# Performance work log

Hardware: AMD Instinct MI355X
Metric: run time of the kernel (lower is better)

Reference implementation:

```python
import jax, jax.numpy as jnp
import numpy as np
import math

B, N, H = 4, 256, 256
D = H  # head_size == hidden_size since num_heads == 1
LN_EPS = 1e-5


def setup_inputs() -> dict:
    key = jax.random.key(0)
    ks = jax.random.split(key, 12)
    s = 0.02
    return {
        "hidden_states": jax.random.normal(ks[0], (B, N, H), jnp.float32),
        "structure_matrix": jax.random.normal(ks[1], (B, N, N, D), jnp.float32),
        "attention_mask": jnp.zeros((B, N), jnp.float32),
        # Linear weights stored as [in, out] (i.e., torch weight transposed)
        "Wq": jax.random.normal(ks[2], (D, D), jnp.float32) * s,
        "bq": jnp.zeros((D,), jnp.float32),
        "Wk": jax.random.normal(ks[3], (H, D), jnp.float32) * s,
        "bk": jnp.zeros((D,), jnp.float32),
        "Wv": jax.random.normal(ks[4], (D, D), jnp.float32) * s,
        "bv": jnp.zeros((D,), jnp.float32),
        "Wo": jax.random.normal(ks[5], (D, H), jnp.float32) * s,
        "bo": jnp.zeros((H,), jnp.float32),
        "ln_gamma": jnp.ones((H,), jnp.float32),
        "ln_beta": jnp.zeros((H,), jnp.float32),
    }


def _layer_norm(x, g, b):
    m = jnp.mean(x, axis=-1, keepdims=True)
    v = jnp.mean(jnp.square(x - m), axis=-1, keepdims=True)
    return g * (x - m) * jax.lax.rsqrt(v + LN_EPS) + b


def reference(hidden_states, structure_matrix, attention_mask,
              Wq, bq, Wk, bk, Wv, bv, Wo, bo, ln_gamma, ln_beta):
    # projections
    q = structure_matrix @ Wq + bq              # [B,L,R,D] with L=R=N
    k = hidden_states @ Wk + bk                 # [B,N,D]
    v = structure_matrix @ Wv + bv              # [B,L,R,D]
    Bq, L, R, Dh = q.shape
    # edge->node attention scores
    scores = jnp.einsum('blrd,bnd->blrn', q, k) / math.sqrt(Dh)
    scores = scores.reshape(Bq, L * R, -1)      # [B, N*N, N]
    # additive pairwise mask
    m2d = (attention_mask[:, :, None] * attention_mask[:, None, :]).reshape(Bq, -1)
    scores = scores + m2d[:, :, None]
    # relu + sum normalization (dropout = identity in eval mode)
    probs = jax.nn.relu(scores)
    probs = probs / jnp.sum(probs + 1e-12, axis=-1, keepdims=True)
    # aggregate edge values to nodes
    context = jnp.einsum('bmn,bmd->bnd', probs, v.reshape(Bq, L * R, Dh))
    out = context @ Wo + bo
    return _layer_norm(out + hidden_states, ln_gamma, ln_beta)
```

## Files before the change

kernel.cpp:

```cpp
#include <hip/hip_runtime.h>
#include <hip/hip_bf16.h>
#include <stdint.h>

#define NB 4
#define NN 256
#define DD 256
#define MM 65536

typedef __attribute__((ext_vector_type(8))) __bf16 bf16x8;
typedef __attribute__((ext_vector_type(4))) __bf16 bf16x4;
typedef __attribute__((ext_vector_type(4))) float f32x4;

__device__ __forceinline__ f32x4 mfma_bf16(bf16x8 a, bf16x8 b, f32x4 c) {
    return __builtin_amdgcn_mfma_f32_16x16x32_bf16(a, b, c, 0, 0, 0);
}

__device__ __forceinline__ size_t fragidx(int row, int col) {
    int nt = row >> 4, ln = row & 15;
    int kk = col >> 5, q = (col >> 3) & 3, e = col & 7;
    return ((size_t)((nt * 8 + kk) * 64 + q * 16 + ln)) * 8 + e;
}


__global__ void zero_kernel(float* __restrict__ p) {
    reinterpret_cast<float4*>(p)[blockIdx.x * 256 + threadIdx.x] =
        make_float4(0.f, 0.f, 0.f, 0.f);
}

__global__ void kkq_kernel(const float* __restrict__ hs, const float* __restrict__ Wk,
                           const float* __restrict__ bk, const float* __restrict__ Wq,
                           const float* __restrict__ bq, __bf16* __restrict__ kqf,
                           float* __restrict__ cb) {
    const int row = blockIdx.x, t = threadIdx.x;
    __shared__ float hr[256];
    __shared__ float kr[256];
    __shared__ float red[256];
    hr[t] = hs[(size_t)row * 256 + t];
    __syncthreads();
    float v = bk[t];
    for (int e = 0; e < 256; ++e)
        v = fmaf(hr[e], Wk[(size_t)e * 256 + t], v);
    kr[t] = v;
    red[t] = v * bq[t];
    __syncthreads();
    float u = 0.f;
    for (int d = 0; d < 256; ++d)
        u = fmaf(Wq[(size_t)t * 256 + d], kr[d], u);
    const int b = row >> 8, n = row & 255;
    kqf[(size_t)b * NN * DD + fragidx(n, t)] = (__bf16)(u * 0.0625f);
    for (int s = 128; s > 0; s >>= 1) {
        if (t < s) red[t] += red[t + s];
        __syncthreads();
    }
    if (t == 0) cb[row] = red[0] * 0.0625f;
}

__global__ void wvoprep_kernel(const float* __restrict__ Wv, const float* __restrict__ Wo,
                               const float* __restrict__ bv, __bf16* __restrict__ wvof,
                               float* __restrict__ bvo) {
    const int h = blockIdx.x, t = threadIdx.x;
    __shared__ float woc[256];
    __shared__ float red[256];
    float wo = Wo[(size_t)t * 256 + h];
    woc[t] = wo;
    red[t] = bv[t] * wo;
    __syncthreads();
    float v = 0.f;
    for (int d = 0; d < 256; ++d)
        v = fmaf(Wv[(size_t)t * 256 + d], woc[d], v);
    wvof[fragidx(h, t)] = (__bf16)v;
    for (int s = 128; s > 0; s >>= 1) {
        if (t < s) red[t] += red[t + s];
        __syncthreads();
    }
    if (t == 0) bvo[h] = red[0];
}

__global__ __launch_bounds__(256, 4)
void phaseA_kernel(const float* __restrict__ S, const __bf16* __restrict__ kqf,
                   const float* __restrict__ cb, const __bf16* __restrict__ wvof,
                   const float* __restrict__ bvo, const float* __restrict__ mask,
                   __bf16* __restrict__ PT, __bf16* __restrict__ VOT,
                   int c0, int CHS) {
    __shared__ __align__(16) __bf16 Tb[8 * 256 * 8];
    const int t = threadIdx.x;
    const int b = blockIdx.y;
    const int w = t >> 6;
    const int lane = t & 63;
    const int q = lane >> 4;
    const int ln = lane & 15;
    const int m0 = c0 + blockIdx.x * 64;
    const int mr = w * 16;

    const float* Ar = S + ((size_t)b * MM + m0 + mr + ln) * DD + q * 8;
    bf16x8 af[8];
#pragma unroll
    for (int kk = 0; kk < 8; ++kk) {
        float4 u0 = *reinterpret_cast<const float4*>(Ar + kk * 32);
        float4 u1 = *reinterpret_cast<const float4*>(Ar + kk * 32 + 4);
        af[kk] = (bf16x8){(__bf16)u0.x, (__bf16)u0.y, (__bf16)u0.z, (__bf16)u0.w,
                          (__bf16)u1.x, (__bf16)u1.y, (__bf16)u1.z, (__bf16)u1.w};
    }

    float m2[4];
#pragma unroll
    for (int r = 0; r < 4; ++r) {
        int mg = m0 + mr + q * 4 + r;
        m2[r] = mask[b * NN + (mg >> 8)] * mask[b * NN + (mg & 255)];
    }

    const int cblk = (mr >> 3) + (q >> 1);
    const int coff = (q & 1) * 4;
    float rs0 = 0.f, rs1 = 0.f, rs2 = 0.f, rs3 = 0.f;
    const __bf16* kqb = kqf + (size_t)b * NN * DD + (size_t)lane * 8;
    const float* cbb = cb + b * NN + ln;
#pragma unroll 2
    for (int nt = 0; nt < 16; ++nt) {
        f32x4 a = {0.f, 0.f, 0.f, 0.f};
        const __bf16* kr = kqb + (size_t)nt * 4096;
#pragma unroll
        for (int kk = 0; kk < 8; ++kk) {
            bf16x8 bf = *reinterpret_cast<const bf16x8*>(kr + kk * 512);
            a = mfma_bf16(af[kk], bf, a);
        }
        float cbv = cbb[nt * 16];
        a.x = fmaxf(a.x + cbv + m2[0], 0.f);
        a.y = fmaxf(a.y + cbv + m2[1], 0.f);
        a.z = fmaxf(a.z + cbv + m2[2], 0.f);
        a.w = fmaxf(a.w + cbv + m2[3], 0.f);
        rs0 += a.x; rs1 += a.y; rs2 += a.z; rs3 += a.w;
        bf16x4 pv = { (__bf16)a.x, (__bf16)a.y, (__bf16)a.z, (__bf16)a.w };
        *reinterpret_cast<bf16x4*>(&Tb[(size_t)(cblk * 256 + nt * 16 + ln) * 8 + coff]) = pv;
    }
#pragma unroll
    for (int off = 1; off < 16; off <<= 1) {
        rs0 += __shfl_xor(rs0, off);
        rs1 += __shfl_xor(rs1, off);
        rs2 += __shfl_xor(rs2, off);
        rs3 += __shfl_xor(rs3, off);
    }
    const float i0 = 1.f / (rs0 + 2.56e-10f);
    const float i1 = 1.f / (rs1 + 2.56e-10f);
    const float i2 = 1.f / (rs2 + 2.56e-10f);
    const float i3 = 1.f / (rs3 + 2.56e-10f);
    __syncthreads();

    {
        __bf16* Pg = PT + (size_t)b * NN * CHS + (size_t)(m0 - c0) * 256;
        const __bf16* Ts = Tb;
#pragma unroll
        for (int it = 0; it < 8; ++it) {
            int idx = it * 256 + t;
            *reinterpret_cast<bf16x8*>(Pg + (size_t)idx * 8) =
                *reinterpret_cast<const bf16x8*>(Ts + (size_t)idx * 8);
        }
    }
    __syncthreads();

    const __bf16* wvb = wvof + (size_t)lane * 8;
#pragma unroll 2
    for (int nt = 0; nt < 16; ++nt) {
        f32x4 a = {0.f, 0.f, 0.f, 0.f};
        const __bf16* wr = wvb + (size_t)nt * 4096;
#pragma unroll
        for (int kk = 0; kk < 8; ++kk) {
            bf16x8 bf = *reinterpret_cast<const bf16x8*>(wr + kk * 512);
            a = mfma_bf16(af[kk], bf, a);
        }
        float bb = bvo[nt * 16 + ln];
        bf16x4 pv = { (__bf16)((a.x + bb) * i0), (__bf16)((a.y + bb) * i1),
                      (__bf16)((a.z + bb) * i2), (__bf16)((a.w + bb) * i3) };
        *reinterpret_cast<bf16x4*>(&Tb[(size_t)(cblk * 256 + nt * 16 + ln) * 8 + coff]) = pv;
    }
    __syncthreads();
    {
        __bf16* Vg = VOT + (size_t)b * NN * CHS + (size_t)(m0 - c0) * 256;
        const __bf16* Ts = Tb;
#pragma unroll
        for (int it = 0; it < 8; ++it) {
            int idx = it * 256 + t;
            *reinterpret_cast<bf16x8*>(Vg + (size_t)idx * 8) =
                *reinterpret_cast<const bf16x8*>(Ts + (size_t)idx * 8);
        }
    }
}

__global__ __launch_bounds__(256, 2)
void phaseB_kernel(const __bf16* __restrict__ PT, const __bf16* __restrict__ VOT,
                   float* __restrict__ accg, int CHS) {
    const int t = threadIdx.x;
    const int b = blockIdx.z;
    const int w = t >> 6;
    const int lane = t & 63;
    const int q = lane >> 4;
    const int ln = lane & 15;
    const int n0 = (blockIdx.x >> 1) * 128 + (w >> 1) * 64;
    const int h0 = (blockIdx.x & 1) * 128 + (w & 1) * 64;
    const int g0 = blockIdx.y * 256;

    f32x4 acc[16];
#pragma unroll
    for (int i = 0; i < 16; ++i) acc[i] = (f32x4){0.f, 0.f, 0.f, 0.f};

    const __bf16* Pb = PT + (size_t)b * NN * CHS;
    const __bf16* Vb = VOT + (size_t)b * NN * CHS;
#pragma unroll 2
    for (int ks = 0; ks < 64; ++ks) {
        const __bf16* Pk = Pb + ((size_t)(g0 + ks * 4 + q) * 256 + n0 + ln) * 8;
        const __bf16* Vk = Vb + ((size_t)(g0 + ks * 4 + q) * 256 + h0 + ln) * 8;
        bf16x8 a[4], bb[4];
#pragma unroll
        for (int i = 0; i < 4; ++i)
            a[i] = *reinterpret_cast<const bf16x8*>(Pk + i * 128);
#pragma unroll
        for (int j = 0; j < 4; ++j)
            bb[j] = *reinterpret_cast<const bf16x8*>(Vk + j * 128);
#pragma unroll
        for (int i = 0; i < 4; ++i)
#pragma unroll
            for (int j = 0; j < 4; ++j)
                acc[i * 4 + j] = mfma_bf16(a[i], bb[j], acc[i * 4 + j]);
    }
    float* og = accg + (size_t)b * NN * DD;
#pragma unroll
    for (int i = 0; i < 4; ++i)
#pragma unroll
        for (int j = 0; j < 4; ++j) {
            f32x4 a = acc[i * 4 + j];
            int n = n0 + i * 16 + q * 4;
            int h = h0 + j * 16 + ln;
            atomicAdd(&og[(size_t)(n + 0) * DD + h], a.x);
            atomicAdd(&og[(size_t)(n + 1) * DD + h], a.y);
            atomicAdd(&og[(size_t)(n + 2) * DD + h], a.z);
            atomicAdd(&og[(size_t)(n + 3) * DD + h], a.w);
        }
}

__global__ void epilogue_kernel(const float* __restrict__ accg, const float* __restrict__ hs,
                                const float* __restrict__ bo, const float* __restrict__ g,
                                const float* __restrict__ be, float* __restrict__ out) {
    const int row = blockIdx.x, t = threadIdx.x;
    __shared__ float red[256];
    const size_t base = (size_t)row * 256;
    float x = accg[base + t] + bo[t] + hs[base + t];
    red[t] = x;
    __syncthreads();
    for (int s = 128; s > 0; s >>= 1) {
        if (t < s) red[t] += red[t + s];
        __syncthreads();
    }
    float mean = red[0] * (1.f / 256.f);
    __syncthreads();
    float d = x - mean;
    red[t] = d * d;
    __syncthreads();
    for (int s = 128; s > 0; s >>= 1) {
        if (t < s) red[t] += red[t + s];
        __syncthreads();
    }
    float var = red[0] * (1.f / 256.f);
    out[base + t] = g[t] * d * rsqrtf(var + 1e-5f) + be[t];
}

extern "C" void kernel_launch(void* const* d_in, const int* in_sizes, int n_in,
                              void* d_out, int out_size, void* d_ws, size_t ws_size,
                              hipStream_t stream) {
    const float* hs   = (const float*)d_in[0];
    const float* S    = (const float*)d_in[1];
    const float* mask = (const float*)d_in[2];
    const float* Wq   = (const float*)d_in[3];
    const float* bq   = (const float*)d_in[4];
    const float* Wk   = (const float*)d_in[5];
    const float* bk   = (const float*)d_in[6];
    const float* Wv   = (const float*)d_in[7];
    const float* bv   = (const float*)d_in[8];
    const float* Wo   = (const float*)d_in[9];
    const float* bo   = (const float*)d_in[10];
    const float* g    = (const float*)d_in[11];
    const float* be   = (const float*)d_in[12];
    float* out = (float*)d_out;

    char* ws = (char*)d_ws;
    size_t off = 0;
    auto alloc = [&](size_t bytes) {
        void* p = ws + off;
        off += (bytes + 255) & ~(size_t)255;
        return p;
    };
    float*  accg = (float*)alloc((size_t)NB * NN * DD * 4);
    __bf16* kqf  = (__bf16*)alloc((size_t)NB * NN * DD * 2);
    float*  cb   = (float*)alloc((size_t)NB * NN * 4);
    __bf16* wvof = (__bf16*)alloc((size_t)NN * DD * 2);
    float*  bvo  = (float*)alloc((size_t)NN * 4);
    size_t rem = ws_size > off ? ws_size - off : 0;
    int CH = MM;
    while (CH > 4096 && (size_t)CH * 4096 + 1024 > rem) CH >>= 1;
    __bf16* PT  = (__bf16*)alloc((size_t)NB * CH * NN * 2);
    __bf16* VOT = (__bf16*)alloc((size_t)NB * CH * NN * 2);

    zero_kernel<<<256, 256, 0, stream>>>(accg);
    kkq_kernel<<<NB * NN, 256, 0, stream>>>(hs, Wk, bk, Wq, bq, kqf, cb);
    wvoprep_kernel<<<NN, 256, 0, stream>>>(Wv, Wo, bv, wvof, bvo);
    for (int c0 = 0; c0 < MM; c0 += CH) {
        phaseA_kernel<<<dim3(CH / 64, NB), 256, 0, stream>>>(S, kqf, cb, wvof, bvo, mask,
                                                             PT, VOT, c0, CH);
        phaseB_kernel<<<dim3(4, CH / 2048, NB), 256, 0, stream>>>(PT, VOT, accg, CH);
    }
    epilogue_kernel<<<NB * NN, 256, 0, stream>>>(accg, hs, bo, g, be, out);
}
```

Before: 670.3 us.

## Give each phaseA wave four row tiles and store fragments directly

Each wave in phaseA now handles 64 rows (four 16-row MFMA tiles) instead of 16, so every loaded kqf/wvof B-fragment feeds four MFMAs. That cuts B-operand global/L2 traffic per row by a factor of four. The shared-memory staging buffer and its __syncthreads are dropped, and results are written straight to the PT/VOT global layout as 8-byte stores. In exchange, register use rises sharply (32 A-fragments plus 16 row sums), occupancy is lowered to 2 blocks, the grid shrinks by four, and the output stores are narrower and less coalesced.

```diff
diff --git a/kernel.cpp b/kernel.cpp
--- a/kernel.cpp
+++ b/kernel.cpp
@@ -76,112 +76,118 @@
     if (t == 0) bvo[h] = red[0];
 }
 
-__global__ __launch_bounds__(256, 4)
+__global__ __launch_bounds__(256, 2)
 void phaseA_kernel(const float* __restrict__ S, const __bf16* __restrict__ kqf,
                    const float* __restrict__ cb, const __bf16* __restrict__ wvof,
                    const float* __restrict__ bvo, const float* __restrict__ mask,
                    __bf16* __restrict__ PT, __bf16* __restrict__ VOT,
                    int c0, int CHS) {
-    __shared__ __align__(16) __bf16 Tb[8 * 256 * 8];
     const int t = threadIdx.x;
     const int b = blockIdx.y;
     const int w = t >> 6;
     const int lane = t & 63;
     const int q = lane >> 4;
     const int ln = lane & 15;
-    const int m0 = c0 + blockIdx.x * 64;
-    const int mr = w * 16;
-
-    const float* Ar = S + ((size_t)b * MM + m0 + mr + ln) * DD + q * 8;
-    bf16x8 af[8];
-#pragma unroll
-    for (int kk = 0; kk < 8; ++kk) {
-        float4 u0 = *reinterpret_cast<const float4*>(Ar + kk * 32);
-        float4 u1 = *reinterpret_cast<const float4*>(Ar + kk * 32 + 4);
-        af[kk] = (bf16x8){(__bf16)u0.x, (__bf16)u0.y, (__bf16)u0.z, (__bf16)u0.w,
-                          (__bf16)u1.x, (__bf16)u1.y, (__bf16)u1.z, (__bf16)u1.w};
-    }
-
-    float m2[4];
-#pragma unroll
-    for (int r = 0; r < 4; ++r) {
-        int mg = m0 + mr + q * 4 + r;
-        m2[r] = mask[b * NN + (mg >> 8)] * mask[b * NN + (mg & 255)];
-    }
-
-    const int cblk = (mr >> 3) + (q >> 1);
-    const int coff = (q & 1) * 4;
-    float rs0 = 0.f, rs1 = 0.f, rs2 = 0.f, rs3 = 0.f;
+    const int mloc = blockIdx.x * 256 + w * 64;
+    const int m0 = c0 + mloc;
+
+    bf16x8 af[4][8];
+#pragma unroll
+    for (int mt = 0; mt < 4; ++mt) {
+        const float* Ar = S + ((size_t)b * MM + m0 + mt * 16 + ln) * DD + q * 8;
+#pragma unroll
+        for (int kk = 0; kk < 8; ++kk) {
+            float4 u0 = *reinterpret_cast<const float4*>(Ar + kk * 32);
+            float4 u1 = *reinterpret_cast<const float4*>(Ar + kk * 32 + 4);
+            af[mt][kk] = (bf16x8){(__bf16)u0.x, (__bf16)u0.y, (__bf16)u0.z, (__bf16)u0.w,
+                                  (__bf16)u1.x, (__bf16)u1.y, (__bf16)u1.z, (__bf16)u1.w};
+        }
+    }
+
+    float m2[16];
+#pragma unroll
+    for (int mt = 0; mt < 4; ++mt)
+#pragma unroll
+        for (int r = 0; r < 4; ++r) {
+            int mg = m0 + mt * 16 + q * 4 + r;
+            m2[mt * 4 + r] = mask[b * NN + (mg >> 8)] * mask[b * NN + (mg & 255)];
+        }
+
+    float rs[16];
+#pragma unroll
+    for (int i = 0; i < 16; ++i) rs[i] = 0.f;
+
     const __bf16* kqb = kqf + (size_t)b * NN * DD + (size_t)lane * 8;
     const float* cbb = cb + b * NN + ln;
+    __bf16* Pb = PT + (size_t)b * NN * CHS;
+    __bf16* Vb = VOT + (size_t)b * NN * CHS;
+    const int mb0 = mloc >> 3;
+    const size_t so = (size_t)ln * 8 + (size_t)(q & 1) * 4;
+
 #pragma unroll 2
     for (int nt = 0; nt < 16; ++nt) {
-        f32x4 a = {0.f, 0.f, 0.f, 0.f};
+        f32x4 a0 = {0.f, 0.f, 0.f, 0.f}, a1 = a0, a2 = a0, a3 = a0;
         const __bf16* kr = kqb + (size_t)nt * 4096;
 #pragma unroll
         for (int kk = 0; kk < 8; ++kk) {
             bf16x8 bf = *reinterpret_cast<const bf16x8*>(kr + kk * 512);
-            a = mfma_bf16(af[kk], bf, a);
-        }
-        float cbv = cbb[nt * 16];
-        a.x = fmaxf(a.x + cbv + m2[0], 0.f);
-        a.y = fmaxf(a.y + cbv + m2[1], 0.f);
-        a.z = fmaxf(a.z + cbv + m2[2], 0.f);
-        a.w = fmaxf(a.w + cbv + m2[3], 0.f);
-        rs0 += a.x; rs1 += a.y; rs2 += a.z; rs3 += a.w;
-        bf16x4 pv = { (__bf16)a.x, (__bf16)a.y, (__bf16)a.z, (__bf16)a.w };
-        *reinterpret_cast<bf16x4*>(&Tb[(size_t)(cblk * 256 + nt * 16 + ln) * 8 + coff]) = pv;
-    }
-#pragma unroll
-    for (int off = 1; off < 16; off <<= 1) {
-        rs0 += __shfl_xor(rs0, off);
-        rs1 += __shfl_xor(rs1, off);
-        rs2 += __shfl_xor(rs2, off);
-        rs3 += __shfl_xor(rs3, off);
-    }
-    const float i0 = 1.f / (rs0 + 2.56e-10f);
-    const float i1 = 1.f / (rs1 + 2.56e-10f);
-    const float i2 = 1.f / (rs2 + 2.56e-10f);
-    const float i3 = 1.f / (rs3 + 2.56e-10f);
-    __syncthreads();
-
-    {
-        __bf16* Pg = PT + (size_t)b * NN * CHS + (size_t)(m0 - c0) * 256;
-        const __bf16* Ts = Tb;
-#pragma unroll
-        for (int it = 0; it < 8; ++it) {
-            int idx = it * 256 + t;
-            *reinterpret_cast<bf16x8*>(Pg + (size_t)idx * 8) =
-                *reinterpret_cast<const bf16x8*>(Ts + (size_t)idx * 8);
-        }
-    }
-    __syncthreads();
+            a0 = mfma_bf16(af[0][kk], bf, a0);
+            a1 = mfma_bf16(af[1][kk], bf, a1);
+            a2 = mfma_bf16(af[2][kk], bf, a2);
+            a3 = mfma_bf16(af[3][kk], bf, a3);
+        }
+        const float cbv = cbb[nt * 16];
+#define PROC_S(mt, A)                                                              \
+        {                                                                          \
+            float x0 = fmaxf(A.x + cbv + m2[mt * 4 + 0], 0.f);                     \
+            float x1 = fmaxf(A.y + cbv + m2[mt * 4 + 1], 0.f);                     \
+            float x2 = fmaxf(A.z + cbv + m2[mt * 4 + 2], 0.f);                     \
+            float x3 = fmaxf(A.w + cbv + m2[mt * 4 + 3], 0.f);                     \
+            rs[mt * 4 + 0] += x0; rs[mt * 4 + 1] += x1;                            \
+            rs[mt * 4 + 2] += x2; rs[mt * 4 + 3] += x3;                            \
+            bf16x4 pv = {(__bf16)x0, (__bf16)x1, (__bf16)x2, (__bf16)x3};          \
+            *reinterpret_cast<bf16x4*>(Pb + (size_t)(mb0 + mt * 2 + (q >> 1)) * 2048 \
+                                       + (size_t)nt * 128 + so) = pv;              \
+        }
+        PROC_S(0, a0) PROC_S(1, a1) PROC_S(2, a2) PROC_S(3, a3)
+#undef PROC_S
+    }
+
+#pragma unroll
+    for (int i = 0; i < 16; ++i) {
+        float v = rs[i];
+        v += __shfl_xor(v, 1);
+        v += __shfl_xor(v, 2);
+        v += __shfl_xor(v, 4);
+        v += __shfl_xor(v, 8);
+        rs[i] = 1.f / (v + 2.56e-10f);
+    }
 
     const __bf16* wvb = wvof + (size_t)lane * 8;
 #pragma unroll 2
     for (int nt = 0; nt < 16; ++nt) {
-        f32x4 a = {0.f, 0.f, 0.f, 0.f};
+        f32x4 a0 = {0.f, 0.f, 0.f, 0.f}, a1 = a0, a2 = a0, a3 = a0;
         const __bf16* wr = wvb + (size_t)nt * 4096;
 #pragma unroll
         for (int kk = 0; kk < 8; ++kk) {
             bf16x8 bf = *reinterpret_cast<const bf16x8*>(wr + kk * 512);
-            a = mfma_bf16(af[kk], bf, a);
-        }
-        float bb = bvo[nt * 16 + ln];
-        bf16x4 pv = { (__bf16)((a.x + bb) * i0), (__bf16)((a.y + bb) * i1),
-                      (__bf16)((a.z + bb) * i2), (__bf16)((a.w + bb) * i3) };
-        *reinterpret_cast<bf16x4*>(&Tb[(size_t)(cblk * 256 + nt * 16 + ln) * 8 + coff]) = pv;
-    }
-    __syncthreads();
-    {
-        __bf16* Vg = VOT + (size_t)b * NN * CHS + (size_t)(m0 - c0) * 256;
-        const __bf16* Ts = Tb;
-#pragma unroll
-        for (int it = 0; it < 8; ++it) {
-            int idx = it * 256 + t;
-            *reinterpret_cast<bf16x8*>(Vg + (size_t)idx * 8) =
-                *reinterpret_cast<const bf16x8*>(Ts + (size_t)idx * 8);
-        }
+            a0 = mfma_bf16(af[0][kk], bf, a0);
+            a1 = mfma_bf16(af[1][kk], bf, a1);
+            a2 = mfma_bf16(af[2][kk], bf, a2);
+            a3 = mfma_bf16(af[3][kk], bf, a3);
+        }
+        const float bb = bvo[nt * 16 + ln];
+#define PROC_V(mt, A)                                                              \
+        {                                                                          \
+            bf16x4 pv = {(__bf16)((A.x + bb) * rs[mt * 4 + 0]),                    \
+                         (__bf16)((A.y + bb) * rs[mt * 4 + 1]),                    \
+                         (__bf16)((A.z + bb) * rs[mt * 4 + 2]),                    \
+                         (__bf16)((A.w + bb) * rs[mt * 4 + 3])};                   \
+            *reinterpret_cast<bf16x4*>(Vb + (size_t)(mb0 + mt * 2 + (q >> 1)) * 2048 \
+                                       + (size_t)nt * 128 + so) = pv;              \
+        }
+        PROC_V(0, a0) PROC_V(1, a1) PROC_V(2, a2) PROC_V(3, a3)
+#undef PROC_V
     }
 }
 
@@ -302,8 +308,8 @@
     kkq_kernel<<<NB * NN, 256, 0, stream>>>(hs, Wk, bk, Wq, bq, kqf, cb);
     wvoprep_kernel<<<NN, 256, 0, stream>>>(Wv, Wo, bv, wvof, bvo);
     for (int c0 = 0; c0 < MM; c0 += CH) {
-        phaseA_kernel<<<dim3(CH / 64, NB), 256, 0, stream>>>(S, kqf, cb, wvof, bvo, mask,
-                                                             PT, VOT, c0, CH);
+        phaseA_kernel<<<dim3(CH / 256, NB), 256, 0, stream>>>(S, kqf, cb, wvof, bvo, mask,
+                                                              PT, VOT, c0, CH);
         phaseB_kernel<<<dim3(4, CH / 2048, NB), 256, 0, stream>>>(PT, VOT, accg, CH);
     }
     epilogue_kernel<<<NB * NN, 256, 0, stream>>>(accg, hs, bo, g, be, out);
```

Result: faster. 641.8 us (-4.2%).

## Aggregate raw structure matrix and apply fused Wv·Wo projection after reduction

Applied to the files above, without the earlier changes.

Phase A no longer multiplies each edge row by the fused Wv·Wo matrix. It writes a bf16 transposed copy of the structure matrix plus normalized probabilities, and accumulates per-node probability sums for the bias term. The fused projection then runs once per node in the epilogue as a 256x256 fp32 matvec, which removes half of the per-edge MFMA work. The costs are a strided transposing gather of S in phase A, atomics for the probability sums, a heavier epilogue, and a smaller default chunk size that launches the kernel loop twice.

```diff
diff --git a/kernel.cpp b/kernel.cpp
--- a/kernel.cpp
+++ b/kernel.cpp
@@ -56,7 +56,7 @@
 }
 
 __global__ void wvoprep_kernel(const float* __restrict__ Wv, const float* __restrict__ Wo,
-                               const float* __restrict__ bv, __bf16* __restrict__ wvof,
+                               const float* __restrict__ bv, float* __restrict__ wvo,
                                float* __restrict__ bvo) {
     const int h = blockIdx.x, t = threadIdx.x;
     __shared__ float woc[256];
@@ -68,7 +68,7 @@
     float v = 0.f;
     for (int d = 0; d < 256; ++d)
         v = fmaf(Wv[(size_t)t * 256 + d], woc[d], v);
-    wvof[fragidx(h, t)] = (__bf16)v;
+    wvo[(size_t)h * 256 + t] = v;
     for (int s = 128; s > 0; s >>= 1) {
         if (t < s) red[t] += red[t + s];
         __syncthreads();
@@ -76,24 +76,23 @@
     if (t == 0) bvo[h] = red[0];
 }
 
-__global__ __launch_bounds__(256, 4)
+__global__ __launch_bounds__(256, 3)
 void phaseA_kernel(const float* __restrict__ S, const __bf16* __restrict__ kqf,
-                   const float* __restrict__ cb, const __bf16* __restrict__ wvof,
-                   const float* __restrict__ bvo, const float* __restrict__ mask,
-                   __bf16* __restrict__ PT, __bf16* __restrict__ VOT,
-                   int c0, int CHS) {
-    __shared__ __align__(16) __bf16 Tb[8 * 256 * 8];
+                   const float* __restrict__ cb, const float* __restrict__ mask,
+                   __bf16* __restrict__ PT, __bf16* __restrict__ ST,
+                   float* __restrict__ wg, int c0, int CHS) {
     const int t = threadIdx.x;
     const int b = blockIdx.y;
     const int w = t >> 6;
     const int lane = t & 63;
     const int q = lane >> 4;
     const int ln = lane & 15;
-    const int m0 = c0 + blockIdx.x * 64;
-    const int mr = w * 16;
-
-    const float* Ar = S + ((size_t)b * MM + m0 + mr + ln) * DD + q * 8;
+    const int mloc = blockIdx.x * 64 + w * 16;
+    const int m0 = c0 + mloc;
+    const int mb0 = mloc >> 3;
+
     bf16x8 af[8];
+    const float* Ar = S + ((size_t)b * MM + m0 + ln) * DD + q * 8;
 #pragma unroll
     for (int kk = 0; kk < 8; ++kk) {
         float4 u0 = *reinterpret_cast<const float4*>(Ar + kk * 32);
@@ -102,19 +101,31 @@
                           (__bf16)u1.x, (__bf16)u1.y, (__bf16)u1.z, (__bf16)u1.w};
     }
 
+    __bf16* Sb = ST + (size_t)b * NN * CHS;
+#pragma unroll
+    for (int it = 0; it < 8; ++it) {
+        const int aa = it >> 2;
+        const int d = (it & 3) * 64 + lane;
+        const float* Sr = S + ((size_t)b * MM + m0 + aa * 8) * DD + d;
+        bf16x8 sv = {(__bf16)Sr[0],      (__bf16)Sr[DD],     (__bf16)Sr[2 * DD],
+                     (__bf16)Sr[3 * DD], (__bf16)Sr[4 * DD], (__bf16)Sr[5 * DD],
+                     (__bf16)Sr[6 * DD], (__bf16)Sr[7 * DD]};
+        *reinterpret_cast<bf16x8*>(Sb + ((size_t)(mb0 + aa) * 256 + d) * 8) = sv;
+    }
+
     float m2[4];
 #pragma unroll
     for (int r = 0; r < 4; ++r) {
-        int mg = m0 + mr + q * 4 + r;
+        int mg = m0 + q * 4 + r;
         m2[r] = mask[b * NN + (mg >> 8)] * mask[b * NN + (mg & 255)];
     }
 
-    const int cblk = (mr >> 3) + (q >> 1);
-    const int coff = (q & 1) * 4;
-    float rs0 = 0.f, rs1 = 0.f, rs2 = 0.f, rs3 = 0.f;
     const __bf16* kqb = kqf + (size_t)b * NN * DD + (size_t)lane * 8;
     const float* cbb = cb + b * NN + ln;
-#pragma unroll 2
+
+    f32x4 p[16];
+    float rs0 = 0.f, rs1 = 0.f, rs2 = 0.f, rs3 = 0.f;
+#pragma unroll
     for (int nt = 0; nt < 16; ++nt) {
         f32x4 a = {0.f, 0.f, 0.f, 0.f};
         const __bf16* kr = kqb + (size_t)nt * 4096;
@@ -123,14 +134,13 @@
             bf16x8 bf = *reinterpret_cast<const bf16x8*>(kr + kk * 512);
             a = mfma_bf16(af[kk], bf, a);
         }
-        float cbv = cbb[nt * 16];
+        const float cbv = cbb[nt * 16];
         a.x = fmaxf(a.x + cbv + m2[0], 0.f);
         a.y = fmaxf(a.y + cbv + m2[1], 0.f);
         a.z = fmaxf(a.z + cbv + m2[2], 0.f);
         a.w = fmaxf(a.w + cbv + m2[3], 0.f);
         rs0 += a.x; rs1 += a.y; rs2 += a.z; rs3 += a.w;
-        bf16x4 pv = { (__bf16)a.x, (__bf16)a.y, (__bf16)a.z, (__bf16)a.w };
-        *reinterpret_cast<bf16x4*>(&Tb[(size_t)(cblk * 256 + nt * 16 + ln) * 8 + coff]) = pv;
+        p[nt] = a;
     }
 #pragma unroll
     for (int off = 1; off < 16; off <<= 1) {
@@ -143,50 +153,24 @@
     const float i1 = 1.f / (rs1 + 2.56e-10f);
     const float i2 = 1.f / (rs2 + 2.56e-10f);
     const float i3 = 1.f / (rs3 + 2.56e-10f);
-    __syncthreads();
-
-    {
-        __bf16* Pg = PT + (size_t)b * NN * CHS + (size_t)(m0 - c0) * 256;
-        const __bf16* Ts = Tb;
-#pragma unroll
-        for (int it = 0; it < 8; ++it) {
-            int idx = it * 256 + t;
-            *reinterpret_cast<bf16x8*>(Pg + (size_t)idx * 8) =
-                *reinterpret_cast<const bf16x8*>(Ts + (size_t)idx * 8);
-        }
-    }
-    __syncthreads();
-
-    const __bf16* wvb = wvof + (size_t)lane * 8;
-#pragma unroll 2
+
+    __bf16* Pb = PT + (size_t)b * NN * CHS;
+    const size_t so = (size_t)ln * 8 + (size_t)(q & 1) * 4;
+#pragma unroll
     for (int nt = 0; nt < 16; ++nt) {
-        f32x4 a = {0.f, 0.f, 0.f, 0.f};
-        const __bf16* wr = wvb + (size_t)nt * 4096;
-#pragma unroll
-        for (int kk = 0; kk < 8; ++kk) {
-            bf16x8 bf = *reinterpret_cast<const bf16x8*>(wr + kk * 512);
-            a = mfma_bf16(af[kk], bf, a);
-        }
-        float bb = bvo[nt * 16 + ln];
-        bf16x4 pv = { (__bf16)((a.x + bb) * i0), (__bf16)((a.y + bb) * i1),
-                      (__bf16)((a.z + bb) * i2), (__bf16)((a.w + bb) * i3) };
-        *reinterpret_cast<bf16x4*>(&Tb[(size_t)(cblk * 256 + nt * 16 + ln) * 8 + coff]) = pv;
-    }
-    __syncthreads();
-    {
-        __bf16* Vg = VOT + (size_t)b * NN * CHS + (size_t)(m0 - c0) * 256;
-        const __bf16* Ts = Tb;
-#pragma unroll
-        for (int it = 0; it < 8; ++it) {
-            int idx = it * 256 + t;
-            *reinterpret_cast<bf16x8*>(Vg + (size_t)idx * 8) =
-                *reinterpret_cast<const bf16x8*>(Ts + (size_t)idx * 8);
-        }
+        float x0 = p[nt].x * i0, x1 = p[nt].y * i1, x2 = p[nt].z * i2, x3 = p[nt].w * i3;
+        bf16x4 pv = {(__bf16)x0, (__bf16)x1, (__bf16)x2, (__bf16)x3};
+        *reinterpret_cast<bf16x4*>(Pb + (size_t)(mb0 + (q >> 1)) * 2048
+                                   + (size_t)nt * 128 + so) = pv;
+        float wn = x0 + x1 + x2 + x3;
+        wn += __shfl_xor(wn, 16);
+        wn += __shfl_xor(wn, 32);
+        if (q == 0) atomicAdd(&wg[b * NN + nt * 16 + ln], wn);
     }
 }
 
 __global__ __launch_bounds__(256, 2)
-void phaseB_kernel(const __bf16* __restrict__ PT, const __bf16* __restrict__ VOT,
+void phaseB_kernel(const __bf16* __restrict__ PT, const __bf16* __restrict__ ST,
                    float* __restrict__ accg, int CHS) {
     const int t = threadIdx.x;
     const int b = blockIdx.z;
@@ -203,7 +187,7 @@
     for (int i = 0; i < 16; ++i) acc[i] = (f32x4){0.f, 0.f, 0.f, 0.f};
 
     const __bf16* Pb = PT + (size_t)b * NN * CHS;
-    const __bf16* Vb = VOT + (size_t)b * NN * CHS;
+    const __bf16* Vb = ST + (size_t)b * NN * CHS;
 #pragma unroll 2
     for (int ks = 0; ks < 64; ++ks) {
         const __bf16* Pk = Pb + ((size_t)(g0 + ks * 4 + q) * 256 + n0 + ln) * 8;
@@ -236,13 +220,22 @@
         }
 }
 
-__global__ void epilogue_kernel(const float* __restrict__ accg, const float* __restrict__ hs,
-                                const float* __restrict__ bo, const float* __restrict__ g,
-                                const float* __restrict__ be, float* __restrict__ out) {
+__global__ void epilogue_kernel(const float* __restrict__ Gg, const float* __restrict__ wg,
+                                const float* __restrict__ wvo, const float* __restrict__ bvo,
+                                const float* __restrict__ hs, const float* __restrict__ bo,
+                                const float* __restrict__ g, const float* __restrict__ be,
+                                float* __restrict__ out) {
     const int row = blockIdx.x, t = threadIdx.x;
+    __shared__ float Grow[256];
     __shared__ float red[256];
     const size_t base = (size_t)row * 256;
-    float x = accg[base + t] + bo[t] + hs[base + t];
+    Grow[t] = Gg[base + t];
+    __syncthreads();
+    float acc = 0.f;
+    const float* wr = wvo + (size_t)t * 256;
+    for (int d = 0; d < 256; ++d)
+        acc = fmaf(Grow[d], wr[d], acc);
+    float x = acc + wg[row] * bvo[t] + bo[t] + hs[base + t];
     red[t] = x;
     __syncthreads();
     for (int s = 128; s > 0; s >>= 1) {
@@ -251,15 +244,15 @@
     }
     float mean = red[0] * (1.f / 256.f);
     __syncthreads();
-    float d = x - mean;
-    red[t] = d * d;
+    float d2 = x - mean;
+    red[t] = d2 * d2;
     __syncthreads();
     for (int s = 128; s > 0; s >>= 1) {
         if (t < s) red[t] += red[t + s];
         __syncthreads();
     }
     float var = red[0] * (1.f / 256.f);
-    out[base + t] = g[t] * d * rsqrtf(var + 1e-5f) + be[t];
+    out[base + t] = g[t] * d2 * rsqrtf(var + 1e-5f) + be[t];
 }
 
 extern "C" void kernel_launch(void* const* d_in, const int* in_sizes, int n_in,
@@ -288,23 +281,24 @@
         return p;
     };
     float*  accg = (float*)alloc((size_t)NB * NN * DD * 4);
+    float*  wg   = (float*)alloc((size_t)NB * NN * 4);
     __bf16* kqf  = (__bf16*)alloc((size_t)NB * NN * DD * 2);
     float*  cb   = (float*)alloc((size_t)NB * NN * 4);
-    __bf16* wvof = (__bf16*)alloc((size_t)NN * DD * 2);
+    float*  wvo  = (float*)alloc((size_t)NN * DD * 4);
     float*  bvo  = (float*)alloc((size_t)NN * 4);
     size_t rem = ws_size > off ? ws_size - off : 0;
-    int CH = MM;
+    int CH = 32768;
     while (CH > 4096 && (size_t)CH * 4096 + 1024 > rem) CH >>= 1;
-    __bf16* PT  = (__bf16*)alloc((size_t)NB * CH * NN * 2);
-    __bf16* VOT = (__bf16*)alloc((size_t)NB * CH * NN * 2);
-
-    zero_kernel<<<256, 256, 0, stream>>>(accg);
+    __bf16* PT = (__bf16*)alloc((size_t)NB * CH * NN * 2);
+    __bf16* ST = (__bf16*)alloc((size_t)NB * CH * NN * 2);
+
+    zero_kernel<<<257, 256, 0, stream>>>(accg);
     kkq_kernel<<<NB * NN, 256, 0, stream>>>(hs, Wk, bk, Wq, bq, kqf, cb);
-    wvoprep_kernel<<<NN, 256, 0, stream>>>(Wv, Wo, bv, wvof, bvo);
+    wvoprep_kernel<<<NN, 256, 0, stream>>>(Wv, Wo, bv, wvo, bvo);
     for (int c0 = 0; c0 < MM; c0 += CH) {
-        phaseA_kernel<<<dim3(CH / 64, NB), 256, 0, stream>>>(S, kqf, cb, wvof, bvo, mask,
-                                                             PT, VOT, c0, CH);
-        phaseB_kernel<<<dim3(4, CH / 2048, NB), 256, 0, stream>>>(PT, VOT, accg, CH);
-    }
-    epilogue_kernel<<<NB * NN, 256, 0, stream>>>(accg, hs, bo, g, be, out);
-}
+        phaseA_kernel<<<dim3(CH / 64, NB), 256, 0, stream>>>(S, kqf, cb, mask,
+                                                             PT, ST, wg, c0, CH);
+        phaseB_kernel<<<dim3(4, CH / 2048, NB), 256, 0, stream>>>(PT, ST, accg, CH);
+    }
+    epilogue_kernel<<<NB * NN, 256, 0, stream>>>(accg, wg, wvo, bvo, hs, bo, g, be, out);
+}
```

After: 1.033 ms. +54.1%, slower.
